# Optimization experiments

Measured on AMD Instinct MI355X. Metric: run time of the kernel, lower is better.

The kernel has to match this reference:

```python
import jax, jax.numpy as jnp
import numpy as np

N, D_IN, HID, N_CLS, E = 100000, 256, 128, 41, 1600000


def setup_inputs() -> dict:
    key = jax.random.key(0)
    ks = jax.random.split(key, 8)
    x = jax.random.normal(ks[0], (N, D_IN), dtype=jnp.float32)
    edge_index = jax.random.randint(ks[1], (2, E), 0, N, dtype=jnp.int64)
    s = 1.0 / np.sqrt(D_IN)
    W1 = jax.random.uniform(ks[2], (D_IN, HID), jnp.float32, -s, s)
    b1 = jnp.zeros((HID,), jnp.float32)
    s2 = 1.0 / np.sqrt(HID)
    W2 = jax.random.uniform(ks[3], (HID, HID), jnp.float32, -s2, s2)
    b2 = jnp.zeros((HID,), jnp.float32)
    lin_w = jax.random.uniform(ks[4], (HID, N_CLS), jnp.float32, -s2, s2)
    lin_b = jnp.zeros((N_CLS,), jnp.float32)
    return {"x": x, "edge_index": edge_index, "W1": W1, "b1": b1,
            "W2": W2, "b2": b2, "lin_w": lin_w, "lin_b": lin_b}


def _gcn_conv(h, src, dst, norm, W, b, n):
    # h: [N, F_in]; transform then gather-scale-scatter (PyG GCNConv order)
    h = h @ W                                   # [N, F_out]
    msg = h[src] * norm[:, None]                # [E+N, F_out]
    return jax.ops.segment_sum(msg, dst, num_segments=n) + b


def reference(x, edge_index, W1, b1, W2, b2, lin_w, lin_b):
    n = x.shape[0]
    loops = jnp.arange(n, dtype=edge_index.dtype)
    src = jnp.concatenate([edge_index[0], loops])  # add self-loops
    dst = jnp.concatenate([edge_index[1], loops])
    # symmetric normalization D^-1/2 (A+I) D^-1/2
    deg = jax.ops.segment_sum(jnp.ones_like(dst, dtype=x.dtype), dst, num_segments=n)
    dis = jnp.where(deg > 0, jax.lax.rsqrt(jnp.maximum(deg, 1.0)), 0.0)
    norm = dis[src] * dis[dst]                   # [E+N]

    x1 = jax.nn.relu(_gcn_conv(x, src, dst, norm, W1, b1, n))   # dropout is identity in eval
    x2 = jax.nn.relu(_gcn_conv(x1, src, dst, norm, W2, b2, n))
    out = (x1 + x2) @ lin_w + lin_b
    return jax.nn.log_softmax(out, axis=1)
```

## Files before the change

### kernel.cpp

```cpp
#include <hip/hip_runtime.h>
#include <math.h>


#define NPAD (1 << 17)
#define CHUNK 1024

typedef __attribute__((ext_vector_type(8))) short short8;
typedef __attribute__((ext_vector_type(4))) float f32x4;

__device__ inline unsigned short f2bf(float f) {
    unsigned u = __builtin_bit_cast(unsigned, f);
    return (unsigned short)((u + 0x7fffu + ((u >> 16) & 1u)) >> 16);
}
__device__ inline float bflo(unsigned u) { return __builtin_bit_cast(float, u << 16); }
__device__ inline float bfhi(unsigned u) { return __builtin_bit_cast(float, u & 0xffff0000u); }


__global__ void mega1(const int* __restrict__ dst, int* __restrict__ cnt, int E, int histB,
                      const float* __restrict__ W1, unsigned short* __restrict__ Wt1,
                      const float* __restrict__ W2, unsigned short* __restrict__ Wt2) {
    int b = blockIdx.x;
    if (b < histB) {
        int e = b * 256 + threadIdx.x;
        if (e < E) atomicAdd(&cnt[dst[e]], 1);
    } else {
        int i = (b - histB) * 256 + threadIdx.x;
        if (i < 256 * 128) {
            int k = i >> 7, nn = i & 127;
            Wt1[nn * 256 + k] = f2bf(W1[i]);
        } else {
            int j = i - 256 * 128;
            if (j < 128 * 128) {
                int k = j >> 7, nn = j & 127;
                Wt2[nn * 128 + k] = f2bf(W2[j]);
            }
        }
    }
}

__global__ void scan_partial(const int* __restrict__ cnt, int* __restrict__ partial, int n) {
    __shared__ int sdata[4];
    int b = blockIdx.x, t = threadIdx.x;
    int base = b * CHUNK;
    int sum = 0;
    for (int i = t; i < CHUNK; i += 256) {
        int idx = base + i;
        if (idx < n) sum += cnt[idx];
    }
#pragma unroll
    for (int off = 32; off > 0; off >>= 1) sum += __shfl_down(sum, off, 64);
    if ((t & 63) == 0) sdata[t >> 6] = sum;
    __syncthreads();
    if (t == 0) partial[b] = sdata[0] + sdata[1] + sdata[2] + sdata[3];
}

__global__ void scan_small(int* partial, int nblk) {
    __shared__ int sm[128];
    int t = threadIdx.x;
    int v = (t < nblk) ? partial[t] : 0;
    int x = v;
    sm[t] = x;
    __syncthreads();
    for (int off = 1; off < 128; off <<= 1) {
        int y = (t >= off) ? sm[t - off] : 0;
        __syncthreads();
        x += y;
        sm[t] = x;
        __syncthreads();
    }
    if (t < nblk) partial[t] = x - v;
}

__global__ void scan_final(const int* __restrict__ cnt, const int* __restrict__ partial,
                           int* __restrict__ offs, int* __restrict__ cursor,
                           float* __restrict__ dis, int n) {
    __shared__ int wsum[4];
    int b = blockIdx.x, t = threadIdx.x;
    int lane = t & 63, w = t >> 6;
    int base = b * CHUNK + t * 4;
    int v[4];
#pragma unroll
    for (int j = 0; j < 4; j++) v[j] = (base + j < n) ? cnt[base + j] : 0;
    int s4 = v[0] + v[1] + v[2] + v[3];
    int inc = s4;
#pragma unroll
    for (int off = 1; off < 64; off <<= 1) {
        int x = __shfl_up(inc, off, 64);
        if (lane >= off) inc += x;
    }
    if (lane == 63) wsum[w] = inc;
    __syncthreads();
    int woff = 0;
    for (int i = 0; i < 4; i++) if (i < w) woff += wsum[i];
    int pos = partial[b] + woff + (inc - s4);
#pragma unroll
    for (int j = 0; j < 4; j++) {
        int idx = base + j;
        if (idx < n) {
            offs[idx] = pos;
            cursor[idx] = pos;
            dis[idx] = rsqrtf((float)(v[j] + 1));
            pos += v[j];
        }
    }
}

template<bool ABF16>
__device__ void gemm_body(int bid, const void* __restrict__ Ap,
                          const unsigned short* __restrict__ Wt,
                          unsigned short* __restrict__ Hb,
                          int n, int K, unsigned short* bs) {
    const int tid = threadIdx.x;
    const int wave = tid >> 6, lane = tid & 63;
    const int quad = lane >> 4, mrow = lane & 15;
    const int arow_g = bid * 64 + wave * 16 + mrow;
    const int arow = arow_g < n ? arow_g : n - 1;

    f32x4 acc[8];
#pragma unroll
    for (int t = 0; t < 8; t++) acc[t] = (f32x4){0.f, 0.f, 0.f, 0.f};

    const float* Af = (const float*)Ap;
    const unsigned short* Ab = (const unsigned short*)Ap;

    for (int kc = 0; kc < K; kc += 128) {
        __syncthreads();
        for (int i = tid; i < 2048; i += 256) {
            int row = i >> 4, c8 = i & 15;
            *(short8*)&bs[row * 136 + c8 * 8] = *(const short8*)&Wt[row * K + kc + c8 * 8];
        }
        __syncthreads();
#pragma unroll
        for (int kt = 0; kt < 128; kt += 32) {
            union { short8 v; unsigned short u[8]; } A;
            if (ABF16) {
                A.v = *(const short8*)&Ab[(size_t)arow * K + kc + kt + quad * 8];
            } else {
                const float* ap = &Af[(size_t)arow * K + kc + kt + quad * 8];
                float4 p0 = *(const float4*)ap;
                float4 p1 = *(const float4*)(ap + 4);
                A.u[0] = f2bf(p0.x); A.u[1] = f2bf(p0.y);
                A.u[2] = f2bf(p0.z); A.u[3] = f2bf(p0.w);
                A.u[4] = f2bf(p1.x); A.u[5] = f2bf(p1.y);
                A.u[6] = f2bf(p1.z); A.u[7] = f2bf(p1.w);
            }
#pragma unroll
            for (int nt = 0; nt < 8; nt++) {
                short8 B = *(const short8*)&bs[(nt * 16 + mrow) * 136 + kt + quad * 8];
                acc[nt] = __builtin_amdgcn_mfma_f32_16x16x32_bf16(A.v, B, acc[nt], 0, 0, 0);
            }
        }
    }
    const int drow0 = bid * 64 + wave * 16 + quad * 4;
#pragma unroll
    for (int r = 0; r < 4; r++) {
        int dr = drow0 + r;
        if (dr < n) {
#pragma unroll
            for (int nt = 0; nt < 8; nt++)
                Hb[(size_t)dr * 128 + nt * 16 + mrow] = f2bf(acc[nt][r]);
        }
    }
}

__global__ __launch_bounds__(256) void mega2(const int* __restrict__ src,
                                             const int* __restrict__ dst,
                                             const float* __restrict__ dis,
                                             int* __restrict__ cursor,
                                             int2* __restrict__ eadj, int E, int permB,
                                             const float* __restrict__ x,
                                             const unsigned short* __restrict__ Wt1,
                                             unsigned short* __restrict__ Hb, int n) {
    __shared__ unsigned short bs[128 * 136];
    int b = blockIdx.x;
    if (b < permB) {
        int e = b * 256 + threadIdx.x;
        if (e < E) {
            int d = dst[e];
            int s = src[e];
            int pos = atomicAdd(&cursor[d], 1);
            eadj[pos] = make_int2(s, __float_as_int(dis[s] * dis[d]));
        }
    } else {
        gemm_body<false>(b - permB, x, Wt1, Hb, n, 256, bs);
    }
}

__global__ __launch_bounds__(256) void gemm2_k(const unsigned short* __restrict__ X1b,
                                               const unsigned short* __restrict__ Wt2,
                                               unsigned short* __restrict__ Hb, int n) {
    __shared__ unsigned short bs[128 * 136];
    gemm_body<true>(blockIdx.x, X1b, Wt2, Hb, n, 128, bs);
}

__global__ __launch_bounds__(256) void gather_h(const unsigned short* __restrict__ Hb,
                                                const int2* __restrict__ eadj,
                                                const int* __restrict__ offs,
                                                const int* __restrict__ cnt,
                                                const float* __restrict__ dis,
                                                const float* __restrict__ bias,
                                                unsigned short* __restrict__ outb,
                                                int n) {
    const int b = blockIdx.x;
    const int xcd = b & 7;
    const int half = xcd >> 2;
    const int nb = ((b >> 3) << 2) | (xcd & 3);
    const int w = threadIdx.x >> 6, lane = threadIdx.x & 63;
    const int grp = lane >> 3, fl = lane & 7;
    const int node = nb * 4 + w;
    const int nd = node < n ? node : n - 1;
    const int st = offs[nd], c = cnt[nd];
    const unsigned short* Hfl = Hb + half * 64 + fl * 8;

    float acc[8];
#pragma unroll
    for (int k = 0; k < 8; k++) acc[k] = 0.f;

    const int2* ep = eadj + st;
    for (int kk = 0; kk < c; kk += 64) {
        int li = kk + lane;
        int2 me = ep[li < c ? li : c - 1];
        float mw = li < c ? __int_as_float(me.y) : 0.f;
        int cend = (c - kk) < 64 ? (c - kk) : 64;

        int   s0 = __shfl(me.x, grp, 64);
        float w0 = __shfl(mw,  grp, 64);
        int   s1 = __shfl(me.x, 8 + grp, 64);
        float w1 = __shfl(mw,  8 + grp, 64);
        uint4 r0 = *(const uint4*)(Hfl + (size_t)s0 * 128);
        uint4 r1 = *(const uint4*)(Hfl + (size_t)s1 * 128);

        for (int j = 0; j < cend; j += 16) {
            int jn = (j + 16 < cend) ? j + 16 : j;
            int   sn0 = __shfl(me.x, jn + grp, 64);
            float wn0 = __shfl(mw,  jn + grp, 64);
            int   sn1 = __shfl(me.x, jn + 8 + grp, 64);
            float wn1 = __shfl(mw,  jn + 8 + grp, 64);
            uint4 rn0 = *(const uint4*)(Hfl + (size_t)sn0 * 128);
            uint4 rn1 = *(const uint4*)(Hfl + (size_t)sn1 * 128);
            acc[0] = fmaf(bflo(r0.x), w0, acc[0]); acc[1] = fmaf(bfhi(r0.x), w0, acc[1]);
            acc[2] = fmaf(bflo(r0.y), w0, acc[2]); acc[3] = fmaf(bfhi(r0.y), w0, acc[3]);
            acc[4] = fmaf(bflo(r0.z), w0, acc[4]); acc[5] = fmaf(bfhi(r0.z), w0, acc[5]);
            acc[6] = fmaf(bflo(r0.w), w0, acc[6]); acc[7] = fmaf(bfhi(r0.w), w0, acc[7]);
            acc[0] = fmaf(bflo(r1.x), w1, acc[0]); acc[1] = fmaf(bfhi(r1.x), w1, acc[1]);
            acc[2] = fmaf(bflo(r1.y), w1, acc[2]); acc[3] = fmaf(bfhi(r1.y), w1, acc[3]);
            acc[4] = fmaf(bflo(r1.z), w1, acc[4]); acc[5] = fmaf(bfhi(r1.z), w1, acc[5]);
            acc[6] = fmaf(bflo(r1.w), w1, acc[6]); acc[7] = fmaf(bfhi(r1.w), w1, acc[7]);
            r0 = rn0; r1 = rn1; w0 = wn0; w1 = wn1;
        }
    }
#pragma unroll
    for (int k = 0; k < 8; k++) {
        acc[k] += __shfl_xor(acc[k], 8, 64);
        acc[k] += __shfl_xor(acc[k], 16, 64);
        acc[k] += __shfl_xor(acc[k], 32, 64);
    }
    float dd = dis[nd], sn = dd * dd;
    uint4 rs = *(const uint4*)(Hfl + (size_t)nd * 128);
    float4 bb0 = ((const float4*)bias)[half * 16 + fl * 2];
    float4 bb1 = ((const float4*)bias)[half * 16 + fl * 2 + 1];
    acc[0] = fmaf(bflo(rs.x), sn, acc[0]) + bb0.x;
    acc[1] = fmaf(bfhi(rs.x), sn, acc[1]) + bb0.y;
    acc[2] = fmaf(bflo(rs.y), sn, acc[2]) + bb0.z;
    acc[3] = fmaf(bfhi(rs.y), sn, acc[3]) + bb0.w;
    acc[4] = fmaf(bflo(rs.z), sn, acc[4]) + bb1.x;
    acc[5] = fmaf(bfhi(rs.z), sn, acc[5]) + bb1.y;
    acc[6] = fmaf(bflo(rs.w), sn, acc[6]) + bb1.z;
    acc[7] = fmaf(bfhi(rs.w), sn, acc[7]) + bb1.w;
#pragma unroll
    for (int k = 0; k < 8; k++) acc[k] = acc[k] > 0.f ? acc[k] : 0.f;

    if (node < n && grp == 0) {
        uint4 pk;
        pk.x = ((unsigned)f2bf(acc[1]) << 16) | (unsigned)f2bf(acc[0]);
        pk.y = ((unsigned)f2bf(acc[3]) << 16) | (unsigned)f2bf(acc[2]);
        pk.z = ((unsigned)f2bf(acc[5]) << 16) | (unsigned)f2bf(acc[4]);
        pk.w = ((unsigned)f2bf(acc[7]) << 16) | (unsigned)f2bf(acc[6]);
        *(uint4*)(outb + (size_t)node * 128 + half * 64 + fl * 8) = pk;
    }
}

__global__ __launch_bounds__(256) void head_k(const unsigned short* __restrict__ x1b,
                                              const unsigned short* __restrict__ x2b,
                                              const float* __restrict__ lw,
                                              const float* __restrict__ lb,
                                              float* __restrict__ out, int n) {
    __shared__ float s[4][128];
    const int w = threadIdx.x >> 6, lane = threadIdx.x & 63;
    const int node = blockIdx.x * 4 + w;
    const int nd = node < n ? node : n - 1;
    unsigned u1 = *(const unsigned*)(x1b + (size_t)nd * 128 + lane * 2);
    unsigned u2 = *(const unsigned*)(x2b + (size_t)nd * 128 + lane * 2);
    s[w][lane * 2]     = bflo(u1) + bflo(u2);
    s[w][lane * 2 + 1] = bfhi(u1) + bfhi(u2);
    bool act = (node < n) && (lane < 41);
    float val = 0.f;
    if (act) {
#pragma unroll 4
        for (int f = 0; f < 128; f++) val = fmaf(s[w][f], lw[f * 41 + lane], val);
        val += lb[lane];
    }
    float m = act ? val : -INFINITY;
#pragma unroll
    for (int off = 32; off > 0; off >>= 1) m = fmaxf(m, __shfl_xor(m, off, 64));
    float e = act ? expf(val - m) : 0.f;
#pragma unroll
    for (int off = 32; off > 0; off >>= 1) e += __shfl_xor(e, off, 64);
    if (act) out[(size_t)node * 41 + lane] = val - m - logf(e);
}

extern "C" void kernel_launch(void* const* d_in, const int* in_sizes, int n_in,
                              void* d_out, int out_size, void* d_ws, size_t ws_size,
                              hipStream_t stream) {
    const float* x  = (const float*)d_in[0];
    const int*   ei = (const int*)d_in[1];
    const float* W1 = (const float*)d_in[2];
    const float* b1 = (const float*)d_in[3];
    const float* W2 = (const float*)d_in[4];
    const float* b2 = (const float*)d_in[5];
    const float* lw = (const float*)d_in[6];
    const float* lb = (const float*)d_in[7];
    float* out = (float*)d_out;

    const int n = in_sizes[0] / 256;
    const int E = in_sizes[1] / 2;
    const int* src = ei;
    const int* dst = ei + E;

    int*   cnt     = (int*)d_ws;
    int*   offs    = cnt + NPAD;
    int*   cursor  = offs + NPAD;
    int*   partial = cursor + NPAD;
    float* dis     = (float*)(partial + 1024);
    size_t Epad    = ((size_t)E + 255) & ~(size_t)255;
    int2*  eadj    = (int2*)(dis + NPAD);
    unsigned short* Wt1 = (unsigned short*)(eadj + Epad);
    unsigned short* Wt2 = Wt1 + 256 * 128;
    unsigned short* Hb  = Wt2 + 128 * 128;
    unsigned short* X1b = Hb + (size_t)n * 128;
    unsigned short* X2b = X1b + (size_t)n * 128;

    const int nscan = (n + CHUNK - 1) / CHUNK;
    const int histB = (E + 255) / 256;
    const int wcastB = (256 * 128 + 128 * 128 + 255) / 256;
    const int permB = histB;
    const int gemmB = (n + 63) / 64;
    const int NB = (n + 3) / 4;
    const int gathB = 8 * ((NB + 3) / 4);

    hipMemsetAsync(cnt, 0, (size_t)n * sizeof(int), stream);

    mega1<<<histB + wcastB, 256, 0, stream>>>(dst, cnt, E, histB, W1, Wt1, W2, Wt2);
    scan_partial<<<nscan, 256, 0, stream>>>(cnt, partial, n);
    scan_small<<<1, 128, 0, stream>>>(partial, nscan);
    scan_final<<<nscan, 256, 0, stream>>>(cnt, partial, offs, cursor, dis, n);

    mega2<<<permB + gemmB, 256, 0, stream>>>(src, dst, dis, cursor, eadj, E, permB,
                                             x, Wt1, Hb, n);

    gather_h<<<gathB, 256, 0, stream>>>(Hb, eadj, offs, cnt, dis, b1, X1b, n);

    gemm2_k<<<gemmB, 256, 0, stream>>>(X1b, Wt2, Hb, n);
    gather_h<<<gathB, 256, 0, stream>>>(Hb, eadj, offs, cnt, dis, b2, X2b, n);

    head_k<<<NB, 256, 0, stream>>>(X1b, X2b, lw, lb, out, n);
}
```

Measured before the change: 616.1 us.

## Split permute from GEMM1 and stage head weights in LDS with persistent blocks

The fused permute+GEMM1 kernel is split back into separate permute_all and gemm1_k launches, so the two no longer run concurrently in one grid. The head kernel becomes a persistent grid-stride kernel with a fixed block count. Each block loads lin_w once into LDS, and the dot product uses four independent accumulators. This cuts repeated global weight reads and the serial FMA dependency chain in the head, at the cost of one extra launch and lost overlap between the atomic permute and the GEMM.

```diff
diff --git a/kernel.cpp b/kernel.cpp
--- a/kernel.cpp
+++ b/kernel.cpp
@@ -105,6 +105,18 @@
     }
 }
 
+__global__ void permute_all(const int* __restrict__ src, const int* __restrict__ dst,
+                            const float* __restrict__ dis,
+                            int* __restrict__ cursor, int2* __restrict__ eadj, int E) {
+    int e = blockIdx.x * 256 + threadIdx.x;
+    if (e < E) {
+        int d = dst[e];
+        int s = src[e];
+        int pos = atomicAdd(&cursor[d], 1);
+        eadj[pos] = make_int2(s, __float_as_int(dis[s] * dis[d]));
+    }
+}
+
 template<bool ABF16>
 __device__ void gemm_body(int bid, const void* __restrict__ Ap,
                           const unsigned short* __restrict__ Wt,
@@ -163,27 +175,11 @@
     }
 }
 
-__global__ __launch_bounds__(256) void mega2(const int* __restrict__ src,
-                                             const int* __restrict__ dst,
-                                             const float* __restrict__ dis,
-                                             int* __restrict__ cursor,
-                                             int2* __restrict__ eadj, int E, int permB,
-                                             const float* __restrict__ x,
-                                             const unsigned short* __restrict__ Wt1,
-                                             unsigned short* __restrict__ Hb, int n) {
+__global__ __launch_bounds__(256) void gemm1_k(const float* __restrict__ x,
+                                               const unsigned short* __restrict__ Wt1,
+                                               unsigned short* __restrict__ Hb, int n) {
     __shared__ unsigned short bs[128 * 136];
-    int b = blockIdx.x;
-    if (b < permB) {
-        int e = b * 256 + threadIdx.x;
-        if (e < E) {
-            int d = dst[e];
-            int s = src[e];
-            int pos = atomicAdd(&cursor[d], 1);
-            eadj[pos] = make_int2(s, __float_as_int(dis[s] * dis[d]));
-        }
-    } else {
-        gemm_body<false>(b - permB, x, Wt1, Hb, n, 256, bs);
-    }
+    gemm_body<false>(blockIdx.x, x, Wt1, Hb, n, 256, bs);
 }
 
 __global__ __launch_bounds__(256) void gemm2_k(const unsigned short* __restrict__ X1b,
@@ -284,29 +280,42 @@
                                               const unsigned short* __restrict__ x2b,
                                               const float* __restrict__ lw,
                                               const float* __restrict__ lb,
-                                              float* __restrict__ out, int n) {
+                                              float* __restrict__ out, int n, int nblk) {
+    __shared__ float lws[128 * 41];
     __shared__ float s[4][128];
-    const int w = threadIdx.x >> 6, lane = threadIdx.x & 63;
-    const int node = blockIdx.x * 4 + w;
-    const int nd = node < n ? node : n - 1;
-    unsigned u1 = *(const unsigned*)(x1b + (size_t)nd * 128 + lane * 2);
-    unsigned u2 = *(const unsigned*)(x2b + (size_t)nd * 128 + lane * 2);
-    s[w][lane * 2]     = bflo(u1) + bflo(u2);
-    s[w][lane * 2 + 1] = bfhi(u1) + bfhi(u2);
-    bool act = (node < n) && (lane < 41);
-    float val = 0.f;
-    if (act) {
-#pragma unroll 4
-        for (int f = 0; f < 128; f++) val = fmaf(s[w][f], lw[f * 41 + lane], val);
-        val += lb[lane];
-    }
-    float m = act ? val : -INFINITY;
-#pragma unroll
-    for (int off = 32; off > 0; off >>= 1) m = fmaxf(m, __shfl_xor(m, off, 64));
-    float e = act ? expf(val - m) : 0.f;
-#pragma unroll
-    for (int off = 32; off > 0; off >>= 1) e += __shfl_xor(e, off, 64);
-    if (act) out[(size_t)node * 41 + lane] = val - m - logf(e);
+    const int tid = threadIdx.x;
+    const int w = tid >> 6, lane = tid & 63;
+    for (int i = tid; i < 128 * 41; i += 256) lws[i] = lw[i];
+    __syncthreads();
+    const float lbv = (lane < 41) ? lb[lane] : 0.f;
+
+    for (int blk = blockIdx.x; blk * 4 < n; blk += nblk) {
+        const int node = blk * 4 + w;
+        const int nd = node < n ? node : n - 1;
+        unsigned u1 = *(const unsigned*)(x1b + (size_t)nd * 128 + lane * 2);
+        unsigned u2 = *(const unsigned*)(x2b + (size_t)nd * 128 + lane * 2);
+        s[w][lane * 2]     = bflo(u1) + bflo(u2);
+        s[w][lane * 2 + 1] = bfhi(u1) + bfhi(u2);
+        const bool act = (node < n) && (lane < 41);
+        float v0 = 0.f, v1 = 0.f, v2 = 0.f, v3 = 0.f;
+        if (act) {
+#pragma unroll 8
+            for (int f = 0; f < 32; f++) {
+                v0 = fmaf(s[w][f],      lws[f * 41 + lane],        v0);
+                v1 = fmaf(s[w][f + 32], lws[(f + 32) * 41 + lane], v1);
+                v2 = fmaf(s[w][f + 64], lws[(f + 64) * 41 + lane], v2);
+                v3 = fmaf(s[w][f + 96], lws[(f + 96) * 41 + lane], v3);
+            }
+        }
+        float val = (v0 + v1) + (v2 + v3) + lbv;
+        float m = act ? val : -INFINITY;
+#pragma unroll
+        for (int off = 32; off > 0; off >>= 1) m = fmaxf(m, __shfl_xor(m, off, 64));
+        float e = act ? expf(val - m) : 0.f;
+#pragma unroll
+        for (int off = 32; off > 0; off >>= 1) e += __shfl_xor(e, off, 64);
+        if (act) out[(size_t)node * 41 + lane] = val - m - logf(e);
+    }
 }
 
 extern "C" void kernel_launch(void* const* d_in, const int* in_sizes, int n_in,
@@ -343,10 +352,10 @@
     const int nscan = (n + CHUNK - 1) / CHUNK;
     const int histB = (E + 255) / 256;
     const int wcastB = (256 * 128 + 128 * 128 + 255) / 256;
-    const int permB = histB;
     const int gemmB = (n + 63) / 64;
     const int NB = (n + 3) / 4;
     const int gathB = 8 * ((NB + 3) / 4);
+    const int headB = 1536;
 
     hipMemsetAsync(cnt, 0, (size_t)n * sizeof(int), stream);
 
@@ -354,14 +363,13 @@
     scan_partial<<<nscan, 256, 0, stream>>>(cnt, partial, n);
     scan_small<<<1, 128, 0, stream>>>(partial, nscan);
     scan_final<<<nscan, 256, 0, stream>>>(cnt, partial, offs, cursor, dis, n);
-
-    mega2<<<permB + gemmB, 256, 0, stream>>>(src, dst, dis, cursor, eadj, E, permB,
-                                             x, Wt1, Hb, n);
-
+    permute_all<<<histB, 256, 0, stream>>>(src, dst, dis, cursor, eadj, E);
+
+    gemm1_k<<<gemmB, 256, 0, stream>>>(x, Wt1, Hb, n);
     gather_h<<<gathB, 256, 0, stream>>>(Hb, eadj, offs, cnt, dis, b1, X1b, n);
 
     gemm2_k<<<gemmB, 256, 0, stream>>>(X1b, Wt2, Hb, n);
     gather_h<<<gathB, 256, 0, stream>>>(Hb, eadj, offs, cnt, dis, b2, X2b, n);
 
-    head_k<<<NB, 256, 0, stream>>>(X1b, X2b, lw, lb, out, n);
-}
+    head_k<<<headB, 256, 0, stream>>>(X1b, X2b, lw, lb, out, n, headB);
+}
```

Result: slower. 640.7 us (+4.0%).
